# Kernel optimization log

Measured on AMD Instinct MI355X. Metric: run time of the kernel, lower is better.

Reference implementation:

```python
import jax, jax.numpy as jnp
import numpy as np

N, E, DIN, H, C = 50000, 800000, 256, 4, 32  # nodes, edges, in_dim, heads, per-head dim
NEG_SLOPE = 0.2  # PyG GATConv default LeakyReLU slope


def setup_inputs() -> dict:
    key = jax.random.key(0)
    ks = jax.random.split(key, 12)
    x = jax.random.normal(ks[0], (N, DIN), jnp.float32)
    edge_index = jax.random.randint(ks[1], (2, E), 0, N, dtype=jnp.int64)
    # layer 1: in=DIN -> heads*C; layer 2: in=H*C -> heads*C (concat=True default)
    W1 = jax.random.normal(ks[2], (DIN, H * C), jnp.float32) / np.sqrt(DIN).astype(np.float32)
    as1 = jax.random.normal(ks[3], (H, C), jnp.float32) * 0.1
    ad1 = jax.random.normal(ks[4], (H, C), jnp.float32) * 0.1
    b1 = jnp.zeros((H * C,), jnp.float32)
    W2 = jax.random.normal(ks[5], (H * C, H * C), jnp.float32) / np.sqrt(H * C).astype(np.float32)
    as2 = jax.random.normal(ks[6], (H, C), jnp.float32) * 0.1
    ad2 = jax.random.normal(ks[7], (H, C), jnp.float32) * 0.1
    b2 = jnp.zeros((H * C,), jnp.float32)
    return {"x": x, "edge_index": edge_index, "W1": W1, "as1": as1, "ad1": ad1,
            "b1": b1, "W2": W2, "as2": as2, "ad2": ad2, "b2": b2}


def gat_conv(x, src, dst, W, a_src, a_dst, b):
    # x: [N, Fin] -> h: [N, H, C]
    n = x.shape[0]
    h = (x @ W).reshape(n, H, C)
    # per-node attention logits [N, H]
    e_src = jnp.einsum('nhc,hc->nh', h, a_src)
    e_dst = jnp.einsum('nhc,hc->nh', h, a_dst)
    # edge-wise logits + segment softmax over destination neighborhoods
    e = jax.nn.leaky_relu(e_src[src] + e_dst[dst], NEG_SLOPE)  # [Et, H]
    m = jax.ops.segment_max(e, dst, num_segments=n)
    ex = jnp.exp(e - m[dst])
    s = jax.ops.segment_sum(ex, dst, num_segments=n)
    alpha = ex / s[dst]  # self-loops guarantee every node has >=1 edge
    # weighted scatter-add aggregation
    out = jax.ops.segment_sum(h[src] * alpha[:, :, None], dst, num_segments=n)
    return out.reshape(n, H * C) + b


def reference(x, edge_index, W1, as1, ad1, b1, W2, as2, ad2, b2):
    n = x.shape[0]
    loop = jnp.arange(n, dtype=edge_index.dtype)
    src = jnp.concatenate([edge_index[0], loop])  # PyG GATConv adds self-loops
    dst = jnp.concatenate([edge_index[1], loop])
    h = jax.nn.elu(gat_conv(x, src, dst, W1, as1, ad1, b1))
    # dropout is a no-op in eval mode (F.dropout with training=False)
    out = jax.nn.elu(gat_conv(h, src, dst, W2, as2, ad2, b2))
    return out
```

## Files before the change

kernel.cpp:

```cpp
#include <hip/hip_runtime.h>
#include <hip/hip_fp16.h>
#include <type_traits>

#define NN 50000
#define NE 800000
#define ET (NE + NN)
#define NEG 0.2f
#define GGRID 782
#define EGRID 3321

typedef __attribute__((ext_vector_type(4))) float f32x4;
typedef __attribute__((ext_vector_type(8))) short s16x8;

#define GLD_LDS16(g, l)                                                        \
  __builtin_amdgcn_global_load_lds(                                            \
      (const __attribute__((address_space(1))) void*)(g),                      \
      (__attribute__((address_space(3))) void*)(l), 16, 0, 0)

__device__ __forceinline__ float lrelu(float x) { return x > 0.0f ? x : NEG * x; }
__device__ __forceinline__ float elu1(float x) { return x > 0.0f ? x : __expf(x) - 1.0f; }
__device__ __forceinline__ unsigned short f2bf(float f) {
  unsigned u = __float_as_uint(f);
  u += 0x7FFFu + ((u >> 16) & 1u);
  return (unsigned short)(u >> 16);
}
__device__ __forceinline__ float bf2f(unsigned short h) {
  return __uint_as_float(((unsigned)h) << 16);
}

__global__ void prep_count_kernel(const float* __restrict__ W1, short* __restrict__ W1h,
                                  short* __restrict__ W1l, const float* __restrict__ W2,
                                  short* __restrict__ W2h, short* __restrict__ W2l,
                                  const int* __restrict__ ei, int* __restrict__ cnt,
                                  int* __restrict__ rank) {
  if (blockIdx.x >= 192) {
    int e = (blockIdx.x - 192) * 256 + threadIdx.x;
    if (e >= ET) return;
    int dst = (e < NE) ? ei[NE + e] : (e - NE);
    rank[e] = atomicAdd(&cnt[dst], 1);
    return;
  }
  int idx = blockIdx.x * 256 + threadIdx.x;
  const float* W; short* Wth; short* Wtl; int Kdim;
  if (idx < 256 * 128) { W = W1; Wth = W1h; Wtl = W1l; Kdim = 256; }
  else {
    idx -= 256 * 128;
    W = W2; Wth = W2h; Wtl = W2l; Kdim = 128;
  }
  int k = idx >> 7, n = idx & 127;
  float w = W[idx];
  unsigned short h = f2bf(w);
  unsigned short l = f2bf(w - bf2f(h));
  Wth[n * Kdim + k] = (short)h;
  Wtl[n * Kdim + k] = (short)l;
}

template<int K, typename AT, bool CSR>
__global__ __launch_bounds__(256) void gemm_mfma(const AT* __restrict__ A,
                                                 const short* __restrict__ Bth,
                                                 const short* __restrict__ Btl,
                                                 const float* __restrict__ a_s,
                                                 const float* __restrict__ a_d,
                                                 __half* __restrict__ outh,
                                                 float* __restrict__ es,
                                                 float* __restrict__ ed,
                                                 const int* __restrict__ ei,
                                                 const int* __restrict__ rank,
                                                 int* __restrict__ colw) {
  if constexpr (CSR) {
    if (blockIdx.x >= GGRID) {
      int e = (blockIdx.x - GGRID) * 256 + threadIdx.x;
      if (e < ET) {
        int src, dst;
        if (e < NE) { src = ei[e]; dst = ei[NE + e]; } else { src = dst = e - NE; }
        int r = rank[e];
        if (r < 128) colw[(dst << 7) + r] = src;
      }
      return;
    }
  }
  constexpr int NSTEP = K / 32;
  __shared__ short Ah[64 * 32], Al[64 * 32];
  __shared__ short Bh[128 * 32], Bl[128 * 32];
  const int tid = threadIdx.x;
  const int lane = tid & 63;
  const int wv = tid >> 6;
  const int wm = wv >> 1, wn = wv & 1;
  const int row0 = blockIdx.x * 64;
  const int srow = tid >> 2;
  const int skc = tid & 3;

  f32x4 acc[2][4];
#pragma unroll
  for (int i = 0; i < 2; ++i)
#pragma unroll
    for (int j = 0; j < 4; ++j) acc[i][j] = (f32x4){0.f, 0.f, 0.f, 0.f};

  for (int s = 0; s < NSTEP; ++s) {
    __syncthreads();
    {
      int grow = row0 + srow; grow = grow < NN ? grow : NN - 1;
      const AT* ap = &A[(size_t)grow * K + s * 32 + skc * 8];
      float xs[8];
      if constexpr (std::is_same_v<AT, float>) {
        float4 x0 = *(const float4*)ap;
        float4 x1 = *(const float4*)(ap + 4);
        xs[0]=x0.x; xs[1]=x0.y; xs[2]=x0.z; xs[3]=x0.w;
        xs[4]=x1.x; xs[5]=x1.y; xs[6]=x1.z; xs[7]=x1.w;
      } else {
        int4 raw = *(const int4*)ap;
        const __half2* hv = (const __half2*)&raw;
#pragma unroll
        for (int q = 0; q < 4; ++q) {
          float2 f = __half22float2(hv[q]);
          xs[2 * q] = f.x; xs[2 * q + 1] = f.y;
        }
      }
      int hi[4], lo[4];
#pragma unroll
      for (int q = 0; q < 4; ++q) {
        unsigned short h0 = f2bf(xs[2 * q]);
        unsigned short l0 = f2bf(xs[2 * q] - bf2f(h0));
        unsigned short h1 = f2bf(xs[2 * q + 1]);
        unsigned short l1 = f2bf(xs[2 * q + 1] - bf2f(h1));
        hi[q] = (int)(((unsigned)h1 << 16) | h0);
        lo[q] = (int)(((unsigned)l1 << 16) | l0);
      }
      *(int4*)&Ah[srow * 32 + skc * 8] = make_int4(hi[0], hi[1], hi[2], hi[3]);
      *(int4*)&Al[srow * 32 + skc * 8] = make_int4(lo[0], lo[1], lo[2], lo[3]);
    }
#pragma unroll
    for (int rr = 0; rr < 2; ++rr) {
      int n = srow + rr * 64;
      const short* gh = &Bth[(size_t)n * K + s * 32 + skc * 8];
      const short* gl = &Btl[(size_t)n * K + s * 32 + skc * 8];
      char* lbh = (char*)Bh + rr * 4096 + wv * 1024;
      char* lbl = (char*)Bl + rr * 4096 + wv * 1024;
      GLD_LDS16(gh, lbh);
      GLD_LDS16(gl, lbl);
    }
    __syncthreads();
    const int fr = lane & 15;
    const int fk = (lane >> 4) * 8;
    s16x8 ah[2], al[2], bh[4], bl[4];
#pragma unroll
    for (int mf = 0; mf < 2; ++mf) {
      int r = wm * 32 + mf * 16 + fr;
      ah[mf] = *(const s16x8*)&Ah[r * 32 + fk];
      al[mf] = *(const s16x8*)&Al[r * 32 + fk];
    }
#pragma unroll
    for (int nf = 0; nf < 4; ++nf) {
      int n = wn * 64 + nf * 16 + fr;
      bh[nf] = *(const s16x8*)&Bh[n * 32 + fk];
      bl[nf] = *(const s16x8*)&Bl[n * 32 + fk];
    }
#pragma unroll
    for (int mf = 0; mf < 2; ++mf)
#pragma unroll
      for (int nf = 0; nf < 4; ++nf) {
        acc[mf][nf] = __builtin_amdgcn_mfma_f32_16x16x32_bf16(ah[mf], bh[nf], acc[mf][nf], 0, 0, 0);
        acc[mf][nf] = __builtin_amdgcn_mfma_f32_16x16x32_bf16(ah[mf], bl[nf], acc[mf][nf], 0, 0, 0);
        acc[mf][nf] = __builtin_amdgcn_mfma_f32_16x16x32_bf16(al[mf], bh[nf], acc[mf][nf], 0, 0, 0);
      }
  }

  const int fr = lane & 15;
  const int fg = lane >> 4;
  float asr[4], adr[4];
#pragma unroll
  for (int nf = 0; nf < 4; ++nf) {
    int c = wn * 64 + nf * 16 + fr;
    asr[nf] = a_s[c]; adr[nf] = a_d[c];
  }
#pragma unroll
  for (int mf = 0; mf < 2; ++mf) {
#pragma unroll
    for (int r = 0; r < 4; ++r) {
      int row = row0 + wm * 32 + mf * 16 + fg * 4 + r;
      float sp0 = acc[mf][0][r] * asr[0] + acc[mf][1][r] * asr[1];
      float sp1 = acc[mf][2][r] * asr[2] + acc[mf][3][r] * asr[3];
      float dp0 = acc[mf][0][r] * adr[0] + acc[mf][1][r] * adr[1];
      float dp1 = acc[mf][2][r] * adr[2] + acc[mf][3][r] * adr[3];
#pragma unroll
      for (int off = 1; off < 16; off <<= 1) {
        sp0 += __shfl_xor(sp0, off); sp1 += __shfl_xor(sp1, off);
        dp0 += __shfl_xor(dp0, off); dp1 += __shfl_xor(dp1, off);
      }
      if (row < NN) {
#pragma unroll
        for (int nf = 0; nf < 4; ++nf)
          outh[(size_t)row * 128 + wn * 64 + nf * 16 + fr] = __float2half(acc[mf][nf][r]);
        if (fr == 0) {
          es[row * 4 + wn * 2 + 0] = sp0;
          es[row * 4 + wn * 2 + 1] = sp1;
          ed[row * 4 + wn * 2 + 0] = dp0;
          ed[row * 4 + wn * 2 + 1] = dp1;
        }
      }
    }
  }
}

template<typename OT>
__global__ __launch_bounds__(128) void agg_fused(const __half* __restrict__ h,
                                                 const float4* __restrict__ es4,
                                                 const float4* __restrict__ ed4,
                                                 const int* __restrict__ cnt,
                                                 const int* __restrict__ col,
                                                 const float* __restrict__ bias,
                                                 OT* __restrict__ out) {
  __shared__ float wc[2][512];
  __shared__ int   cc[2][128];
  int wid = (blockIdx.x * 128 + threadIdx.x) >> 6;
  if (wid >= NN) return;
  const int lane = threadIdx.x & 63;
  const int wv = (threadIdx.x >> 6) & 1;
  int deg = cnt[wid];
  deg = deg < 128 ? deg : 128;
  const int start = wid << 7;
  const float4 edv = ed4[wid];
  const char* hb = (const char*)h;

  const bool v0 = lane < deg, v1 = lane + 64 < deg;
  int c0 = 0, c1 = 0;
  float4 e0, e1;
  if (v0) { c0 = col[start + lane]; e0 = es4[c0]; }
  if (v1) { c1 = col[start + lane + 64]; e1 = es4[c1]; }
  float s0 = 0.f, s1 = 0.f, s2 = 0.f, s3 = 0.f;
  float4 p0, p1;
  if (v0) {
    p0.x = __expf(lrelu(e0.x + edv.x)); p0.y = __expf(lrelu(e0.y + edv.y));
    p0.z = __expf(lrelu(e0.z + edv.z)); p0.w = __expf(lrelu(e0.w + edv.w));
    s0 += p0.x; s1 += p0.y; s2 += p0.z; s3 += p0.w;
  }
  if (v1) {
    p1.x = __expf(lrelu(e1.x + edv.x)); p1.y = __expf(lrelu(e1.y + edv.y));
    p1.z = __expf(lrelu(e1.z + edv.z)); p1.w = __expf(lrelu(e1.w + edv.w));
    s0 += p1.x; s1 += p1.y; s2 += p1.z; s3 += p1.w;
  }
#pragma unroll
  for (int off = 32; off; off >>= 1) {
    s0 += __shfl_xor(s0, off); s1 += __shfl_xor(s1, off);
    s2 += __shfl_xor(s2, off); s3 += __shfl_xor(s3, off);
  }
  const float i0 = 1.0f / s0, i1 = 1.0f / s1, i2 = 1.0f / s2, i3 = 1.0f / s3;
  if (v0) {
    float4 w; w.x = p0.x * i0; w.y = p0.y * i1; w.z = p0.z * i2; w.w = p0.w * i3;
    *(float4*)&wc[wv][lane * 4] = w;
    cc[wv][lane] = c0 << 8;
  }
  if (v1) {
    float4 w; w.x = p1.x * i0; w.y = p1.y * i1; w.z = p1.z * i2; w.w = p1.w * i3;
    *(float4*)&wc[wv][(lane + 64) * 4] = w;
    cc[wv][lane + 64] = c1 << 8;
  }
  if (lane == 0 && (deg & 1)) {
    cc[wv][deg] = cc[wv][0];
    float4 z = {0.f, 0.f, 0.f, 0.f};
    *(float4*)&wc[wv][deg * 4] = z;
  }

  const int half_ = lane >> 5;
  const int fl = lane & 31;
  const int hd2 = fl >> 3;
  const int fb = fl << 3;
  float a0 = 0.f, a1 = 0.f, a2 = 0.f, a3 = 0.f;
  const int degR = (deg + 1) & ~1;
  int jj = 0;
  for (; jj + 8 <= degR; jj += 8) {
    int off[4]; float w[4];
#pragma unroll
    for (int u = 0; u < 4; ++u) {
      int e = jj + 2 * u + half_;
      off[u] = cc[wv][e];
      w[u] = wc[wv][e * 4 + hd2];
    }
    int2 q[4];
#pragma unroll
    for (int u = 0; u < 4; ++u) q[u] = *(const int2*)(hb + off[u] + fb);
#pragma unroll
    for (int u = 0; u < 4; ++u) {
      float2 f0 = __half22float2(*(const __half2*)&q[u].x);
      float2 f1 = __half22float2(*(const __half2*)&q[u].y);
      a0 = fmaf(f0.x, w[u], a0); a1 = fmaf(f0.y, w[u], a1);
      a2 = fmaf(f1.x, w[u], a2); a3 = fmaf(f1.y, w[u], a3);
    }
  }
  for (; jj < degR; jj += 2) {
    int e = jj + half_;
    int off = cc[wv][e];
    float w = wc[wv][e * 4 + hd2];
    int2 q = *(const int2*)(hb + off + fb);
    float2 f0 = __half22float2(*(const __half2*)&q.x);
    float2 f1 = __half22float2(*(const __half2*)&q.y);
    a0 = fmaf(f0.x, w, a0); a1 = fmaf(f0.y, w, a1);
    a2 = fmaf(f1.x, w, a2); a3 = fmaf(f1.y, w, a3);
  }
  a0 += __shfl_xor(a0, 32); a1 += __shfl_xor(a1, 32);
  a2 += __shfl_xor(a2, 32); a3 += __shfl_xor(a3, 32);

  float4 bs = *(const float4*)&bias[fl * 4];
  if (half_ == 0) {
    float o0 = elu1(a0 + bs.x), o1 = elu1(a1 + bs.y);
    float o2 = elu1(a2 + bs.z), o3 = elu1(a3 + bs.w);
    if constexpr (std::is_same_v<OT, float>) {
      float4 o; o.x = o0; o.y = o1; o.z = o2; o.w = o3;
      *(float4*)&out[(size_t)wid * 128 + fl * 4] = o;
    } else {
      __half2 h01 = __floats2half2_rn(o0, o1);
      __half2 h23 = __floats2half2_rn(o2, o3);
      int2 pk; pk.x = *(int*)&h01; pk.y = *(int*)&h23;
      *(int2*)&out[(size_t)wid * 128 + fl * 4] = pk;
    }
  }
}

extern "C" void kernel_launch(void* const* d_in, const int* in_sizes, int n_in,
                              void* d_out, int out_size, void* d_ws, size_t ws_size,
                              hipStream_t stream) {
  const float* x   = (const float*)d_in[0];
  const int*   ei  = (const int*)d_in[1];
  const float* W1  = (const float*)d_in[2];
  const float* as1 = (const float*)d_in[3];
  const float* ad1 = (const float*)d_in[4];
  const float* b1  = (const float*)d_in[5];
  const float* W2  = (const float*)d_in[6];
  const float* as2 = (const float*)d_in[7];
  const float* ad2 = (const float*)d_in[8];
  const float* b2  = (const float*)d_in[9];

  char* ws = (char*)d_ws;
  __half* h     = (__half*)(ws);
  float*  es    = (float*) (ws + 12800000);
  float*  ed    = (float*) (ws + 13600000);
  int*    cnt   = (int*)   (ws + 14400000);
  int*    col   = (int*)   (ws + 14600064);
  int*    rank  = (int*)   (ws + 40200064);
  short*  wt1h  = (short*) (ws + 43600064);
  short*  wt1l  = (short*) (ws + 43665600);
  short*  wt2h  = (short*) (ws + 43731136);
  short*  wt2l  = (short*) (ws + 43763904);
  __half* h2    = (__half*)d_out;

  hipMemsetAsync(cnt, 0, NN * sizeof(int), stream);

  prep_count_kernel<<<192 + EGRID, 256, 0, stream>>>(W1, wt1h, wt1l, W2, wt2h, wt2l,
                                                     ei, cnt, rank);

  int ngrid = (NN + 1) / 2;

  gemm_mfma<256, float, true><<<GGRID + EGRID, 256, 0, stream>>>(
      x, wt1h, wt1l, as1, ad1, h, es, ed, ei, rank, col);

  agg_fused<__half><<<ngrid, 128, 0, stream>>>(h, (const float4*)es, (const float4*)ed,
                                               cnt, col, b1, h2);

  gemm_mfma<128, __half, false><<<GGRID, 256, 0, stream>>>(
      h2, wt2h, wt2l, as2, ad2, h, es, ed, nullptr, nullptr, nullptr);

  agg_fused<float><<<ngrid, 128, 0, stream>>>(h, (const float4*)es, (const float4*)ed,
                                              cnt, col, b2, (float*)d_out);
}
```

Before: 166.0 us.

## Double-buffer LDS tiles in GEMM to overlap next-step loads with MFMA

```diff
diff --git a/kernel.cpp b/kernel.cpp
--- a/kernel.cpp
+++ b/kernel.cpp
@@ -80,8 +80,8 @@
     }
   }
   constexpr int NSTEP = K / 32;
-  __shared__ short Ah[64 * 32], Al[64 * 32];
-  __shared__ short Bh[128 * 32], Bl[128 * 32];
+  __shared__ short Ah[2][64 * 32], Al[2][64 * 32];
+  __shared__ short Bh[2][128 * 32], Bl[2][128 * 32];
   const int tid = threadIdx.x;
   const int lane = tid & 63;
   const int wv = tid >> 6;
@@ -89,71 +89,91 @@
   const int row0 = blockIdx.x * 64;
   const int srow = tid >> 2;
   const int skc = tid & 3;
-
-  f32x4 acc[2][4];
-#pragma unroll
-  for (int i = 0; i < 2; ++i)
-#pragma unroll
-    for (int j = 0; j < 4; ++j) acc[i][j] = (f32x4){0.f, 0.f, 0.f, 0.f};
-
-  for (int s = 0; s < NSTEP; ++s) {
-    __syncthreads();
-    {
-      int grow = row0 + srow; grow = grow < NN ? grow : NN - 1;
-      const AT* ap = &A[(size_t)grow * K + s * 32 + skc * 8];
-      float xs[8];
-      if constexpr (std::is_same_v<AT, float>) {
-        float4 x0 = *(const float4*)ap;
-        float4 x1 = *(const float4*)(ap + 4);
-        xs[0]=x0.x; xs[1]=x0.y; xs[2]=x0.z; xs[3]=x0.w;
-        xs[4]=x1.x; xs[5]=x1.y; xs[6]=x1.z; xs[7]=x1.w;
-      } else {
-        int4 raw = *(const int4*)ap;
-        const __half2* hv = (const __half2*)&raw;
-#pragma unroll
-        for (int q = 0; q < 4; ++q) {
-          float2 f = __half22float2(hv[q]);
-          xs[2 * q] = f.x; xs[2 * q + 1] = f.y;
-        }
-      }
-      int hi[4], lo[4];
+  int grow = row0 + srow; grow = grow < NN ? grow : NN - 1;
+  const AT* aptr = &A[(size_t)grow * K + skc * 8];
+
+  float4 xa0, xa1;
+  int4 xraw;
+
+  auto loadA = [&](int s) {
+    if constexpr (std::is_same_v<AT, float>) {
+      xa0 = *(const float4*)(aptr + s * 32);
+      xa1 = *(const float4*)(aptr + s * 32 + 4);
+    } else {
+      xraw = *(const int4*)(aptr + s * 32);
+    }
+  };
+  auto writeA = [&](int b) {
+    float xs[8];
+    if constexpr (std::is_same_v<AT, float>) {
+      xs[0]=xa0.x; xs[1]=xa0.y; xs[2]=xa0.z; xs[3]=xa0.w;
+      xs[4]=xa1.x; xs[5]=xa1.y; xs[6]=xa1.z; xs[7]=xa1.w;
+    } else {
+      const __half2* hv = (const __half2*)&xraw;
 #pragma unroll
       for (int q = 0; q < 4; ++q) {
-        unsigned short h0 = f2bf(xs[2 * q]);
-        unsigned short l0 = f2bf(xs[2 * q] - bf2f(h0));
-        unsigned short h1 = f2bf(xs[2 * q + 1]);
-        unsigned short l1 = f2bf(xs[2 * q + 1] - bf2f(h1));
-        hi[q] = (int)(((unsigned)h1 << 16) | h0);
-        lo[q] = (int)(((unsigned)l1 << 16) | l0);
-      }
-      *(int4*)&Ah[srow * 32 + skc * 8] = make_int4(hi[0], hi[1], hi[2], hi[3]);
-      *(int4*)&Al[srow * 32 + skc * 8] = make_int4(lo[0], lo[1], lo[2], lo[3]);
-    }
+        float2 f = __half22float2(hv[q]);
+        xs[2 * q] = f.x; xs[2 * q + 1] = f.y;
+      }
+    }
+    int hi[4], lo[4];
+#pragma unroll
+    for (int q = 0; q < 4; ++q) {
+      unsigned short h0 = f2bf(xs[2 * q]);
+      unsigned short l0 = f2bf(xs[2 * q] - bf2f(h0));
+      unsigned short h1 = f2bf(xs[2 * q + 1]);
+      unsigned short l1 = f2bf(xs[2 * q + 1] - bf2f(h1));
+      hi[q] = (int)(((unsigned)h1 << 16) | h0);
+      lo[q] = (int)(((unsigned)l1 << 16) | l0);
+    }
+    *(int4*)&Ah[b][srow * 32 + skc * 8] = make_int4(hi[0], hi[1], hi[2], hi[3]);
+    *(int4*)&Al[b][srow * 32 + skc * 8] = make_int4(lo[0], lo[1], lo[2], lo[3]);
+  };
+  auto stageB = [&](int s, int b) {
 #pragma unroll
     for (int rr = 0; rr < 2; ++rr) {
       int n = srow + rr * 64;
       const short* gh = &Bth[(size_t)n * K + s * 32 + skc * 8];
       const short* gl = &Btl[(size_t)n * K + s * 32 + skc * 8];
-      char* lbh = (char*)Bh + rr * 4096 + wv * 1024;
-      char* lbl = (char*)Bl + rr * 4096 + wv * 1024;
+      char* lbh = (char*)&Bh[b][0] + rr * 4096 + wv * 1024;
+      char* lbl = (char*)&Bl[b][0] + rr * 4096 + wv * 1024;
       GLD_LDS16(gh, lbh);
       GLD_LDS16(gl, lbl);
     }
-    __syncthreads();
-    const int fr = lane & 15;
-    const int fk = (lane >> 4) * 8;
+  };
+
+  f32x4 acc[2][4];
+#pragma unroll
+  for (int i = 0; i < 2; ++i)
+#pragma unroll
+    for (int j = 0; j < 4; ++j) acc[i][j] = (f32x4){0.f, 0.f, 0.f, 0.f};
+
+  const int fr = lane & 15;
+  const int fk = (lane >> 4) * 8;
+
+  stageB(0, 0);
+  loadA(0);
+  writeA(0);
+  __syncthreads();
+
+  for (int s = 0; s < NSTEP; ++s) {
+    const int cur = s & 1;
+    if (s + 1 < NSTEP) {
+      stageB(s + 1, cur ^ 1);
+      loadA(s + 1);
+    }
     s16x8 ah[2], al[2], bh[4], bl[4];
 #pragma unroll
     for (int mf = 0; mf < 2; ++mf) {
       int r = wm * 32 + mf * 16 + fr;
-      ah[mf] = *(const s16x8*)&Ah[r * 32 + fk];
-      al[mf] = *(const s16x8*)&Al[r * 32 + fk];
+      ah[mf] = *(const s16x8*)&Ah[cur][r * 32 + fk];
+      al[mf] = *(const s16x8*)&Al[cur][r * 32 + fk];
     }
 #pragma unroll
     for (int nf = 0; nf < 4; ++nf) {
       int n = wn * 64 + nf * 16 + fr;
-      bh[nf] = *(const s16x8*)&Bh[n * 32 + fk];
-      bl[nf] = *(const s16x8*)&Bl[n * 32 + fk];
+      bh[nf] = *(const s16x8*)&Bh[cur][n * 32 + fk];
+      bl[nf] = *(const s16x8*)&Bl[cur][n * 32 + fk];
     }
 #pragma unroll
     for (int mf = 0; mf < 2; ++mf)
@@ -163,9 +183,10 @@
         acc[mf][nf] = __builtin_amdgcn_mfma_f32_16x16x32_bf16(ah[mf], bl[nf], acc[mf][nf], 0, 0, 0);
         acc[mf][nf] = __builtin_amdgcn_mfma_f32_16x16x32_bf16(al[mf], bh[nf], acc[mf][nf], 0, 0, 0);
       }
-  }
-
-  const int fr = lane & 15;
+    if (s + 1 < NSTEP) writeA(cur ^ 1);
+    __syncthreads();
+  }
+
   const int fg = lane >> 4;
   float asr[4], adr[4];
 #pragma unroll
```

After: 177.9 us. 1.07x slower.
